# Optimization experiments

Measured on AMD Instinct MI355X. Metric: run time of the kernel, lower is better.

Reference implementation:

```python
import jax, jax.numpy as jnp
import numpy as np

B, H, S, D = 2, 12, 1024, 128
KQ, KK = 6, 11  # per-head conv kernel over (query, key) score plane


def setup_inputs() -> dict:
    key = jax.random.key(0)
    kq, kk, kv, kw = jax.random.split(key, 4)
    Q = jax.random.normal(kq, (B, H, S, D), dtype=jnp.float32)
    K = jax.random.normal(kk, (B, H, S, D), dtype=jnp.float32)
    V = jax.random.normal(kv, (B, H, S, D), dtype=jnp.float32)
    W = jax.random.normal(kw, (H, KQ, KK), dtype=jnp.float32) * 0.1
    return {"Q": Q, "K": K, "V": V, "W": W}


def reference(Q, K, V, W):
    # causal=True, softmax_scale = 1/sqrt(head_dim)  (module defaults)
    b, h, s, d = Q.shape
    _, kq, kk = W.shape
    pad_q = kq - 1            # causal padding along the query axis
    pad_k = (kk - 1) // 2     # 'same' padding along the key axis
    scale = 1.0 / np.sqrt(d).astype(np.float32)

    # Raw QK^T scores: [b, h, s_q, s_k]
    scores = jnp.einsum('bhqd,bhkd->bhqk', Q, K)

    # Causal: zero out future keys before the conv so the kernel cannot mix
    # in future information (matches the `causal` flag passed into the
    # fused qk_conv kernel; out-of-range tiles load as 0 in the Triton code).
    tril = jnp.tril(jnp.ones((s, s), dtype=bool))
    scores = jnp.where(tril[None, None], scores, 0.0)

    # Per-head 2D conv over the (q, k) plane: grouped conv with H groups,
    # kernel W[h] applied to head h's score map. Cross-correlation (PyTorch
    # conv semantics == lax.conv_general_dilated without kernel flip).
    conv = jax.lax.conv_general_dilated(
        scores,                      # [b, h, s, s] as NCHW
        W[:, None, :, :],            # [h, 1, kq, kk] as OIHW, groups=h
        window_strides=(1, 1),
        padding=((pad_q, 0), (pad_k, pad_k)),
        feature_group_count=h,
        dimension_numbers=('NCHW', 'OIHW', 'NCHW'),
    )

    # Scale, re-apply causal mask with the kernel's -1e6 fill, softmax, @V.
    logits = conv * scale + jnp.where(tril[None, None], 0.0, -1000000.0)
    P = jax.nn.softmax(logits, axis=-1)
    O = jnp.einsum('bhqk,bhkd->bhqd', P, V)
    return O
```

## Files before the change

kernel.cpp:

```cpp
#include <hip/hip_runtime.h>
#include <hip/hip_bf16.h>
#include <math.h>

#define B_ 2
#define H_ 12
#define S_ 1024
#define D_ 128
#define TQ 32
#define TK 32
#define NW 4
#define SCALE 0.08838834764831843f

#define QPAD 16
#define QROWS (S_ + QPAD)
#define KPAD 16
#define KROWS (KPAD + S_ + 16)

typedef __attribute__((ext_vector_type(8))) short short8;
typedef __attribute__((ext_vector_type(4))) float floatx4;

__device__ __forceinline__ float b2f(short s) {
    unsigned int x = ((unsigned int)(unsigned short)s) << 16;
    return __builtin_bit_cast(float, x);
}
__device__ __forceinline__ unsigned short f2b(float f) {
    return __builtin_bit_cast(unsigned short, __float2bfloat16(f));
}

__global__ __launch_bounds__(256) void cvt_pad_kernel(
    const float* __restrict__ src, unsigned short* __restrict__ dst,
    int rows_total)
{
    int idx = blockIdx.x * 256 + threadIdx.x;
    size_t e0 = (size_t)idx * 4;
    int bh = (int)(e0 / ((size_t)rows_total * D_));
    int rem = (int)(e0 - (size_t)bh * rows_total * D_);
    int r = rem / D_;
    int d = rem - r * D_;
    int sr = r - 16;
    float4 v = make_float4(0.f, 0.f, 0.f, 0.f);
    if (sr >= 0 && sr < S_)
        v = *(const float4*)(src + ((size_t)bh * S_ + sr) * D_ + d);
    ushort4 o;
    o.x = f2b(v.x); o.y = f2b(v.y); o.z = f2b(v.z); o.w = f2b(v.w);
    *(ushort4*)(dst + ((size_t)bh * rows_total + r) * D_ + d) = o;
}

__global__ __launch_bounds__(256) void vt_kernel(
    const float* __restrict__ V, unsigned short* __restrict__ Vt)
{
    __shared__ float ls[32][33];
    int b = blockIdx.x;
    int dt = b & 3; int kt = (b >> 2) & 31; int bh = b >> 7;
    int t = threadIdx.x;
    int lk = t >> 3, ld = (t & 7) * 4;
    float4 v = *(const float4*)(V + ((size_t)bh * S_ + kt * 32 + lk) * D_ + dt * 32 + ld);
    ls[lk][ld + 0] = v.x; ls[lk][ld + 1] = v.y; ls[lk][ld + 2] = v.z; ls[lk][ld + 3] = v.w;
    __syncthreads();
    int lk2 = t >> 3, lc = (t & 7) * 4;
    ushort4 o;
    o.x = f2b(ls[lc + 0][lk2]); o.y = f2b(ls[lc + 1][lk2]);
    o.z = f2b(ls[lc + 2][lk2]); o.w = f2b(ls[lc + 3][lk2]);
    *(ushort4*)(Vt + ((size_t)bh * D_ + dt * 32 + lk2) * S_ + kt * 32 + lc) = o;
}

__global__ __launch_bounds__(256, 2) void conv_attn_mfma(
    const unsigned short* __restrict__ Qp,
    const unsigned short* __restrict__ Kp,
    const unsigned short* __restrict__ Vt,
    const float* __restrict__ W,
    float* __restrict__ O)
{
    __shared__ __align__(16) union {
        unsigned short sc[NW][48][72];
        float oacc[32][132];
    } u;
    __shared__ float m_all[NW][32], l_all[NW][32], ms_s[32], inv_s[32];

    const int tid = threadIdx.x;
    const int wv = tid >> 6;
    const int ln = tid & 63;
    const int l15 = ln & 15;
    const int qd = ln >> 4;

    const int bid = blockIdx.x;
    const int bh = bid % (B_ * H_);
    const int qt = (S_ / TQ - 1) - bid / (B_ * H_);
    const int h = bh % H_;
    const int q0 = qt * TQ;

    const unsigned short* Qb = Qp + (size_t)bh * QROWS * D_;
    const unsigned short* Kb = Kp + (size_t)bh * KROWS * D_;
    const unsigned short* Vb = Vt + (size_t)bh * D_ * S_;
    const float* Wh = W + h * 66;

    short8 qf[3][4];
    #pragma unroll
    for (int mt = 0; mt < 3; ++mt) {
        const unsigned short* row = Qb + (size_t)(q0 + mt * 16 + l15) * D_;
        #pragma unroll
        for (int kc = 0; kc < 4; ++kc)
            qf[mt][kc] = *(const short8*)(row + kc * 32 + qd * 8);
    }

    floatx4 acc[2][8];
    #pragma unroll
    for (int mt = 0; mt < 2; ++mt)
        #pragma unroll
        for (int nt = 0; nt < 8; ++nt)
            acc[mt][nt] = (floatx4){0.f, 0.f, 0.f, 0.f};
    float m_run[2] = {-INFINITY, -INFINITY};
    float l_run[2] = {0.f, 0.f};

    const int nkt = qt + 1;
    for (int kt = wv; kt < nkt; kt += NW) {
        const int k0 = kt * TK;

        short8 vf[8];
        #pragma unroll
        for (int nt = 0; nt < 8; ++nt)
            vf[nt] = *(const short8*)(Vb + (size_t)(nt * 16 + l15) * S_ + k0 + qd * 8);

        #pragma unroll
        for (int nt = 0; nt < 3; ++nt) {
            const unsigned short* krow = Kb + (size_t)(k0 + 8 + nt * 16 + l15) * D_;
            short8 kf[4];
            #pragma unroll
            for (int kc = 0; kc < 4; ++kc)
                kf[kc] = *(const short8*)(krow + kc * 32 + qd * 8);
            #pragma unroll
            for (int mt = 0; mt < 3; ++mt) {
                floatx4 s = {0.f, 0.f, 0.f, 0.f};
                #pragma unroll
                for (int kc = 0; kc < 4; ++kc)
                    s = __builtin_amdgcn_mfma_f32_16x16x32_bf16(qf[mt][kc], kf[kc], s, 0, 0, 0);
                const int qrow = q0 - 16 + mt * 16 + qd * 4;
                const int kcol = k0 - 8 + nt * 16 + l15;
                #pragma unroll
                for (int reg = 0; reg < 4; ++reg) {
                    float v = (kcol <= qrow + reg) ? s[reg] : 0.f;
                    u.sc[wv][mt * 16 + qd * 4 + reg][nt * 16 + l15] = f2b(v);
                }
            }
        }

        float pl[2][8];
        #pragma unroll
        for (int mt2 = 0; mt2 < 2; ++mt2)
            #pragma unroll
            for (int jj = 0; jj < 8; ++jj) pl[mt2][jj] = 0.f;
        #pragma unroll
        for (int i = 0; i < 6; ++i) {
            const unsigned short* r0 = &u.sc[wv][l15 + 11 + i][qd * 8];
            const unsigned short* r1 = &u.sc[wv][l15 + 27 + i][qd * 8];
            short8 h0 = *(const short8*)(r0);
            short8 h1 = *(const short8*)(r0 + 8);
            short8 h2 = *(const short8*)(r0 + 16);
            short8 g0 = *(const short8*)(r1);
            short8 g1 = *(const short8*)(r1 + 8);
            short8 g2 = *(const short8*)(r1 + 16);
            float x0[24], x1[24];
            #pragma unroll
            for (int m = 0; m < 8; ++m) {
                x0[m] = b2f(h0[m]); x0[8 + m] = b2f(h1[m]); x0[16 + m] = b2f(h2[m]);
                x1[m] = b2f(g0[m]); x1[8 + m] = b2f(g1[m]); x1[16 + m] = b2f(g2[m]);
            }
            #pragma unroll
            for (int j = 0; j < 11; ++j) {
                const float w = Wh[i * 11 + j];
                #pragma unroll
                for (int jj = 0; jj < 8; ++jj) {
                    pl[0][jj] += w * x0[3 + j + jj];
                    pl[1][jj] += w * x1[3 + j + jj];
                }
            }
        }

        float al[2];
        short8 pfrag[2];
        #pragma unroll
        for (int mt2 = 0; mt2 < 2; ++mt2) {
            const int qrow = q0 + l15 + 16 * mt2;
            float lg[8];
            float mx = -1e30f;
            #pragma unroll
            for (int jj = 0; jj < 8; ++jj) {
                const int kcol = k0 + qd * 8 + jj;
                lg[jj] = (kcol <= qrow) ? pl[mt2][jj] * SCALE : -1e30f;
                mx = fmaxf(mx, lg[jj]);
            }
            mx = fmaxf(mx, __shfl_xor(mx, 16));
            mx = fmaxf(mx, __shfl_xor(mx, 32));
            const float nm = fmaxf(m_run[mt2], mx);
            al[mt2] = __expf(m_run[mt2] - nm);
            float sum = 0.f;
            short8 pb;
            #pragma unroll
            for (int jj = 0; jj < 8; ++jj) {
                float p = __expf(lg[jj] - nm);
                sum += p;
                pb[jj] = (short)f2b(p);
            }
            sum += __shfl_xor(sum, 16);
            sum += __shfl_xor(sum, 32);
            l_run[mt2] = l_run[mt2] * al[mt2] + sum;
            m_run[mt2] = nm;
            pfrag[mt2] = pb;
        }

        #pragma unroll
        for (int mt = 0; mt < 2; ++mt) {
            #pragma unroll
            for (int reg = 0; reg < 4; ++reg) {
                const float af = __shfl(al[mt], qd * 4 + reg, 64);
                #pragma unroll
                for (int nt = 0; nt < 8; ++nt)
                    acc[mt][nt][reg] *= af;
            }
        }

        #pragma unroll
        for (int nt = 0; nt < 8; ++nt)
            #pragma unroll
            for (int mt = 0; mt < 2; ++mt)
                acc[mt][nt] = __builtin_amdgcn_mfma_f32_16x16x32_bf16(pfrag[mt], vf[nt], acc[mt][nt], 0, 0, 0);
    }

    if (qd == 0) {
        m_all[wv][l15] = m_run[0]; m_all[wv][l15 + 16] = m_run[1];
        l_all[wv][l15] = l_run[0]; l_all[wv][l15 + 16] = l_run[1];
    }
    __syncthreads();
    if (tid < 32) {
        float ms = -INFINITY;
        #pragma unroll
        for (int w = 0; w < NW; ++w) ms = fmaxf(ms, m_all[w][tid]);
        float ls = 0.f;
        #pragma unroll
        for (int w = 0; w < NW; ++w) ls += __expf(m_all[w][tid] - ms) * l_all[w][tid];
        ms_s[tid] = ms;
        inv_s[tid] = 1.f / ls;
    }
    __syncthreads();
    for (int w = 0; w < NW; ++w) {
        if (wv == w) {
            #pragma unroll
            for (int mt = 0; mt < 2; ++mt) {
                #pragma unroll
                for (int reg = 0; reg < 4; ++reg) {
                    const int row = mt * 16 + qd * 4 + reg;
                    const float f = __expf(m_all[wv][row] - ms_s[row]);
                    #pragma unroll
                    for (int nt = 0; nt < 8; ++nt) {
                        const float val = acc[mt][nt][reg] * f;
                        if (w == 0) u.oacc[row][nt * 16 + l15] = val;
                        else        u.oacc[row][nt * 16 + l15] += val;
                    }
                }
            }
        }
        __syncthreads();
    }

    {
        const int r = tid >> 3;
        const int c0 = (tid & 7) * 16;
        const float inv = inv_s[r];
        float* orow = O + ((size_t)bh * S_ + q0 + r) * D_ + c0;
        #pragma unroll
        for (int g = 0; g < 4; ++g) {
            float4 o;
            o.x = u.oacc[r][c0 + g * 4 + 0] * inv;
            o.y = u.oacc[r][c0 + g * 4 + 1] * inv;
            o.z = u.oacc[r][c0 + g * 4 + 2] * inv;
            o.w = u.oacc[r][c0 + g * 4 + 3] * inv;
            *(float4*)(orow + g * 4) = o;
        }
    }
}

extern "C" void kernel_launch(void* const* d_in, const int* in_sizes, int n_in,
                              void* d_out, int out_size, void* d_ws, size_t ws_size,
                              hipStream_t stream) {
    const float* Q = (const float*)d_in[0];
    const float* K = (const float*)d_in[1];
    const float* V = (const float*)d_in[2];
    const float* W = (const float*)d_in[3];
    float* O = (float*)d_out;

    unsigned short* Qp = (unsigned short*)d_ws;
    unsigned short* Kp = (unsigned short*)((char*)d_ws + 6389760);
    unsigned short* Vt = (unsigned short*)((char*)d_ws + 12877824);

    cvt_pad_kernel<<<dim3((B_ * H_ * QROWS * D_) / 1024), dim3(256), 0, stream>>>(Q, Qp, QROWS);
    cvt_pad_kernel<<<dim3((B_ * H_ * KROWS * D_) / 1024), dim3(256), 0, stream>>>(K, Kp, KROWS);
    vt_kernel<<<dim3(B_ * H_ * (S_ / 32) * (D_ / 32)), dim3(256), 0, stream>>>(V, Vt);

    conv_attn_mfma<<<dim3(B_ * H_ * (S_ / TQ)), dim3(256), 0, stream>>>(Qp, Kp, Vt, W, O);
}
```

Baseline: 200.8 us.

## Merge prep kernels, stage Q in LDS, keep conv scores in fp32

```diff
diff --git a/kernel.cpp b/kernel.cpp
--- a/kernel.cpp
+++ b/kernel.cpp
@@ -11,57 +11,62 @@
 #define NW 4
 #define SCALE 0.08838834764831843f
 
-#define QPAD 16
-#define QROWS (S_ + QPAD)
-#define KPAD 16
-#define KROWS (KPAD + S_ + 16)
+#define QROWS (S_ + 16)
+#define KROWS (16 + S_ + 16)
+
+#define QBLK 3120
+#define KBLK 3168
+#define VBLK 3072
 
 typedef __attribute__((ext_vector_type(8))) short short8;
 typedef __attribute__((ext_vector_type(4))) float floatx4;
 
-__device__ __forceinline__ float b2f(short s) {
-    unsigned int x = ((unsigned int)(unsigned short)s) << 16;
-    return __builtin_bit_cast(float, x);
-}
 __device__ __forceinline__ unsigned short f2b(float f) {
     return __builtin_bit_cast(unsigned short, __float2bfloat16(f));
 }
 
-__global__ __launch_bounds__(256) void cvt_pad_kernel(
-    const float* __restrict__ src, unsigned short* __restrict__ dst,
-    int rows_total)
-{
-    int idx = blockIdx.x * 256 + threadIdx.x;
-    size_t e0 = (size_t)idx * 4;
-    int bh = (int)(e0 / ((size_t)rows_total * D_));
-    int rem = (int)(e0 - (size_t)bh * rows_total * D_);
-    int r = rem / D_;
-    int d = rem - r * D_;
-    int sr = r - 16;
-    float4 v = make_float4(0.f, 0.f, 0.f, 0.f);
-    if (sr >= 0 && sr < S_)
-        v = *(const float4*)(src + ((size_t)bh * S_ + sr) * D_ + d);
-    ushort4 o;
-    o.x = f2b(v.x); o.y = f2b(v.y); o.z = f2b(v.z); o.w = f2b(v.w);
-    *(ushort4*)(dst + ((size_t)bh * rows_total + r) * D_ + d) = o;
-}
-
-__global__ __launch_bounds__(256) void vt_kernel(
-    const float* __restrict__ V, unsigned short* __restrict__ Vt)
+__global__ __launch_bounds__(256) void prep_kernel(
+    const float* __restrict__ Q, const float* __restrict__ K,
+    const float* __restrict__ V,
+    unsigned short* __restrict__ Qp, unsigned short* __restrict__ Kp,
+    unsigned short* __restrict__ Vt)
 {
     __shared__ float ls[32][33];
-    int b = blockIdx.x;
-    int dt = b & 3; int kt = (b >> 2) & 31; int bh = b >> 7;
-    int t = threadIdx.x;
-    int lk = t >> 3, ld = (t & 7) * 4;
-    float4 v = *(const float4*)(V + ((size_t)bh * S_ + kt * 32 + lk) * D_ + dt * 32 + ld);
-    ls[lk][ld + 0] = v.x; ls[lk][ld + 1] = v.y; ls[lk][ld + 2] = v.z; ls[lk][ld + 3] = v.w;
-    __syncthreads();
-    int lk2 = t >> 3, lc = (t & 7) * 4;
-    ushort4 o;
-    o.x = f2b(ls[lc + 0][lk2]); o.y = f2b(ls[lc + 1][lk2]);
-    o.z = f2b(ls[lc + 2][lk2]); o.w = f2b(ls[lc + 3][lk2]);
-    *(ushort4*)(Vt + ((size_t)bh * D_ + dt * 32 + lk2) * S_ + kt * 32 + lc) = o;
+    const int bid = blockIdx.x;
+    const int tid = threadIdx.x;
+    if (bid < QBLK) {
+        int e0 = (bid * 256 + tid) * 4;
+        int bh = e0 / (QROWS * D_);
+        int rem = e0 - bh * (QROWS * D_);
+        int r = rem >> 7, d = rem & 127;
+        int sr = r - 16;
+        float4 v = make_float4(0.f, 0.f, 0.f, 0.f);
+        if (sr >= 0 && sr < S_) v = *(const float4*)(Q + ((size_t)bh * S_ + sr) * D_ + d);
+        ushort4 o; o.x = f2b(v.x); o.y = f2b(v.y); o.z = f2b(v.z); o.w = f2b(v.w);
+        *(ushort4*)(Qp + ((size_t)bh * QROWS + r) * D_ + d) = o;
+    } else if (bid < QBLK + KBLK) {
+        int e0 = ((bid - QBLK) * 256 + tid) * 4;
+        int bh = e0 / (KROWS * D_);
+        int rem = e0 - bh * (KROWS * D_);
+        int r = rem >> 7, d = rem & 127;
+        int sr = r - 16;
+        float4 v = make_float4(0.f, 0.f, 0.f, 0.f);
+        if (sr >= 0 && sr < S_) v = *(const float4*)(K + ((size_t)bh * S_ + sr) * D_ + d);
+        ushort4 o; o.x = f2b(v.x); o.y = f2b(v.y); o.z = f2b(v.z); o.w = f2b(v.w);
+        *(ushort4*)(Kp + ((size_t)bh * KROWS + r) * D_ + d) = o;
+    } else {
+        int b = bid - (QBLK + KBLK);
+        int dt = b & 3; int kt = (b >> 2) & 31; int bh = b >> 7;
+        int lk = tid >> 3, ld = (tid & 7) * 4;
+        float4 v = *(const float4*)(V + ((size_t)bh * S_ + kt * 32 + lk) * D_ + dt * 32 + ld);
+        ls[lk][ld + 0] = v.x; ls[lk][ld + 1] = v.y; ls[lk][ld + 2] = v.z; ls[lk][ld + 3] = v.w;
+        __syncthreads();
+        int lk2 = tid >> 3, lc = (tid & 7) * 4;
+        ushort4 o;
+        o.x = f2b(ls[lc + 0][lk2]); o.y = f2b(ls[lc + 1][lk2]);
+        o.z = f2b(ls[lc + 2][lk2]); o.w = f2b(ls[lc + 3][lk2]);
+        *(ushort4*)(Vt + ((size_t)bh * D_ + dt * 32 + lk2) * S_ + kt * 32 + lc) = o;
+    }
 }
 
 __global__ __launch_bounds__(256, 2) void conv_attn_mfma(
@@ -71,8 +76,9 @@
     const float* __restrict__ W,
     float* __restrict__ O)
 {
+    __shared__ __align__(16) unsigned short Qs[48][136];
     __shared__ __align__(16) union {
-        unsigned short sc[NW][48][72];
+        float sc[NW][48][52];
         float oacc[32][132];
     } u;
     __shared__ float m_all[NW][32], l_all[NW][32], ms_s[32], inv_s[32];
@@ -94,14 +100,11 @@
     const unsigned short* Vb = Vt + (size_t)bh * D_ * S_;
     const float* Wh = W + h * 66;
 
-    short8 qf[3][4];
-    #pragma unroll
-    for (int mt = 0; mt < 3; ++mt) {
-        const unsigned short* row = Qb + (size_t)(q0 + mt * 16 + l15) * D_;
-        #pragma unroll
-        for (int kc = 0; kc < 4; ++kc)
-            qf[mt][kc] = *(const short8*)(row + kc * 32 + qd * 8);
-    }
+    for (int idx = tid; idx < 48 * 16; idx += 256) {
+        int r = idx >> 4, c8 = (idx & 15) * 8;
+        *(short8*)&Qs[r][c8] = *(const short8*)(Qb + (size_t)(q0 + r) * D_ + c8);
+    }
+    __syncthreads();
 
     floatx4 acc[2][8];
     #pragma unroll
@@ -116,30 +119,32 @@
     for (int kt = wv; kt < nkt; kt += NW) {
         const int k0 = kt * TK;
 
-        short8 vf[8];
-        #pragma unroll
-        for (int nt = 0; nt < 8; ++nt)
-            vf[nt] = *(const short8*)(Vb + (size_t)(nt * 16 + l15) * S_ + k0 + qd * 8);
-
-        #pragma unroll
-        for (int nt = 0; nt < 3; ++nt) {
-            const unsigned short* krow = Kb + (size_t)(k0 + 8 + nt * 16 + l15) * D_;
-            short8 kf[4];
-            #pragma unroll
-            for (int kc = 0; kc < 4; ++kc)
-                kf[kc] = *(const short8*)(krow + kc * 32 + qd * 8);
-            #pragma unroll
-            for (int mt = 0; mt < 3; ++mt) {
-                floatx4 s = {0.f, 0.f, 0.f, 0.f};
+        {
+            short8 qf[3][4];
+            #pragma unroll
+            for (int mt = 0; mt < 3; ++mt)
                 #pragma unroll
                 for (int kc = 0; kc < 4; ++kc)
-                    s = __builtin_amdgcn_mfma_f32_16x16x32_bf16(qf[mt][kc], kf[kc], s, 0, 0, 0);
-                const int qrow = q0 - 16 + mt * 16 + qd * 4;
-                const int kcol = k0 - 8 + nt * 16 + l15;
-                #pragma unroll
-                for (int reg = 0; reg < 4; ++reg) {
-                    float v = (kcol <= qrow + reg) ? s[reg] : 0.f;
-                    u.sc[wv][mt * 16 + qd * 4 + reg][nt * 16 + l15] = f2b(v);
+                    qf[mt][kc] = *(const short8*)&Qs[mt * 16 + l15][kc * 32 + qd * 8];
+            #pragma unroll
+            for (int nt = 0; nt < 3; ++nt) {
+                const unsigned short* krow = Kb + (size_t)(k0 + 8 + nt * 16 + l15) * D_;
+                short8 kf[4];
+                #pragma unroll
+                for (int kc = 0; kc < 4; ++kc)
+                    kf[kc] = *(const short8*)(krow + kc * 32 + qd * 8);
+                #pragma unroll
+                for (int mt = 0; mt < 3; ++mt) {
+                    floatx4 s = {0.f, 0.f, 0.f, 0.f};
+                    #pragma unroll
+                    for (int kc = 0; kc < 4; ++kc)
+                        s = __builtin_amdgcn_mfma_f32_16x16x32_bf16(qf[mt][kc], kf[kc], s, 0, 0, 0);
+                    const int qrow = q0 - 16 + mt * 16 + qd * 4;
+                    const int kcol = k0 - 8 + nt * 16 + l15;
+                    #pragma unroll
+                    for (int reg = 0; reg < 4; ++reg)
+                        u.sc[wv][mt * 16 + qd * 4 + reg][nt * 16 + l15] =
+                            (kcol <= qrow + reg) ? s[reg] : 0.f;
                 }
             }
         }
@@ -150,28 +155,25 @@
             #pragma unroll
             for (int jj = 0; jj < 8; ++jj) pl[mt2][jj] = 0.f;
         #pragma unroll
-        for (int i = 0; i < 6; ++i) {
-            const unsigned short* r0 = &u.sc[wv][l15 + 11 + i][qd * 8];
-            const unsigned short* r1 = &u.sc[wv][l15 + 27 + i][qd * 8];
-            short8 h0 = *(const short8*)(r0);
-            short8 h1 = *(const short8*)(r0 + 8);
-            short8 h2 = *(const short8*)(r0 + 16);
-            short8 g0 = *(const short8*)(r1);
-            short8 g1 = *(const short8*)(r1 + 8);
-            short8 g2 = *(const short8*)(r1 + 16);
-            float x0[24], x1[24];
-            #pragma unroll
-            for (int m = 0; m < 8; ++m) {
-                x0[m] = b2f(h0[m]); x0[8 + m] = b2f(h1[m]); x0[16 + m] = b2f(h2[m]);
-                x1[m] = b2f(g0[m]); x1[8 + m] = b2f(g1[m]); x1[16 + m] = b2f(g2[m]);
-            }
-            #pragma unroll
-            for (int j = 0; j < 11; ++j) {
-                const float w = Wh[i * 11 + j];
-                #pragma unroll
-                for (int jj = 0; jj < 8; ++jj) {
-                    pl[0][jj] += w * x0[3 + j + jj];
-                    pl[1][jj] += w * x1[3 + j + jj];
+        for (int mt2 = 0; mt2 < 2; ++mt2) {
+            #pragma unroll
+            for (int i = 0; i < 6; ++i) {
+                const float* rp = &u.sc[wv][l15 + 11 + 16 * mt2 + i][qd * 8];
+                float4 a0 = ((const float4*)rp)[0];
+                float4 a1 = ((const float4*)rp)[1];
+                float4 a2 = ((const float4*)rp)[2];
+                float4 a3 = ((const float4*)rp)[3];
+                float4 a4 = ((const float4*)rp)[4];
+                float2 a5 = *(const float2*)(rp + 20);
+                float win[22] = {a0.x, a0.y, a0.z, a0.w, a1.x, a1.y, a1.z, a1.w,
+                                 a2.x, a2.y, a2.z, a2.w, a3.x, a3.y, a3.z, a3.w,
+                                 a4.x, a4.y, a4.z, a4.w, a5.x, a5.y};
+                #pragma unroll
+                for (int j = 0; j < 11; ++j) {
+                    const float w = Wh[i * 11 + j];
+                    #pragma unroll
+                    for (int jj = 0; jj < 8; ++jj)
+                        pl[mt2][jj] = fmaf(w, win[3 + j + jj], pl[mt2][jj]);
                 }
             }
         }
@@ -219,11 +221,17 @@
             }
         }
 
-        #pragma unroll
-        for (int nt = 0; nt < 8; ++nt)
-            #pragma unroll
-            for (int mt = 0; mt < 2; ++mt)
-                acc[mt][nt] = __builtin_amdgcn_mfma_f32_16x16x32_bf16(pfrag[mt], vf[nt], acc[mt][nt], 0, 0, 0);
+        {
+            short8 vf[8];
+            #pragma unroll
+            for (int nt = 0; nt < 8; ++nt)
+                vf[nt] = *(const short8*)(Vb + (size_t)(nt * 16 + l15) * S_ + k0 + qd * 8);
+            #pragma unroll
+            for (int nt = 0; nt < 8; ++nt)
+                #pragma unroll
+                for (int mt = 0; mt < 2; ++mt)
+                    acc[mt][nt] = __builtin_amdgcn_mfma_f32_16x16x32_bf16(pfrag[mt], vf[nt], acc[mt][nt], 0, 0, 0);
+        }
     }
 
     if (qd == 0) {
@@ -292,9 +300,6 @@
     unsigned short* Kp = (unsigned short*)((char*)d_ws + 6389760);
     unsigned short* Vt = (unsigned short*)((char*)d_ws + 12877824);
 
-    cvt_pad_kernel<<<dim3((B_ * H_ * QROWS * D_) / 1024), dim3(256), 0, stream>>>(Q, Qp, QROWS);
-    cvt_pad_kernel<<<dim3((B_ * H_ * KROWS * D_) / 1024), dim3(256), 0, stream>>>(K, Kp, KROWS);
-    vt_kernel<<<dim3(B_ * H_ * (S_ / 32) * (D_ / 32)), dim3(256), 0, stream>>>(V, Vt);
-
+    prep_kernel<<<dim3(QBLK + KBLK + VBLK), dim3(256), 0, stream>>>(Q, K, V, Qp, Kp, Vt);
     conv_attn_mfma<<<dim3(B_ * H_ * (S_ / TQ)), dim3(256), 0, stream>>>(Qp, Kp, Vt, W, O);
 }
```

After: 209.4 us. 1.04x slower.
